# Kernel optimization log

Measured on AMD Instinct MI355X. Metric: run time of the kernel, lower is better.

The kernel has to match this reference:

```python
import jax, jax.numpy as jnp
import numpy as np

B, C, K, H, W = 32, 256, 64, 56, 56


def setup_inputs() -> dict:
    key = jax.random.key(0)
    k1, k2, k3, k4 = jax.random.split(key, 4)
    main_out = jax.random.normal(k1, (B, C, H, W), dtype=jnp.float32)
    dup_out = jax.random.normal(k2, (B, K, H, W), dtype=jnp.float32)
    # buffers: per-channel valid ranges with min <= max
    min_vals = -jnp.abs(jax.random.uniform(k3, (C,), dtype=jnp.float32))
    max_vals = jnp.abs(jax.random.uniform(k4, (C,), dtype=jnp.float32)) + 0.5
    vulnerable_idx = jnp.arange(K, dtype=jnp.int32)  # first K channels are duplicated
    return {
        "main_out": main_out,
        "dup_out": dup_out,
        "min_vals": min_vals,
        "max_vals": max_vals,
        "vulnerable_idx": vulnerable_idx,
    }


def reference(main_out, dup_out, min_vals, max_vals, vulnerable_idx):
    # nan->0 (inf handled like torch.nan_to_num defaults: clamped to finite max)
    main = jnp.nan_to_num(main_out, nan=0.0)
    dup = jnp.nan_to_num(dup_out, nan=0.0)

    lo = min_vals[None, :, None, None]   # [1,C,1,1]
    hi = max_vals[None, :, None, None]

    # non-vulnerable path: zero out-of-range values (applied to all channels,
    # then vulnerable channels are overwritten below)
    out = jnp.where((main >= lo) & (main <= hi), main, jnp.zeros((), main.dtype))

    # vulnerable channels: compare main vs duplicate
    m = main[:, vulnerable_idx]          # [B,K,H,W]
    d = dup                              # [B,K,H,W]
    lov = min_vals[vulnerable_idx][None, :, None, None]
    hiv = max_vals[vulnerable_idx][None, :, None, None]
    m_valid = (m >= lov) & (m <= hiv)
    d_valid = (d >= lov) & (d <= hiv)

    # both valid and differing -> min(m,d); only d valid -> d;
    # m valid (alone or both-equal) -> m; neither -> 0
    res = jnp.where(
        m_valid & d_valid & (m != d), jnp.minimum(m, d),
        jnp.where(d_valid & ~m_valid, d,
                  jnp.where(m_valid, m, jnp.zeros((), m.dtype))))

    return out.at[:, vulnerable_idx].set(res)
```

## Files before the change

kernel.cpp:

```cpp
#include <hip/hip_runtime.h>

constexpr int BB  = 32;
constexpr int CC  = 256;
constexpr int HWN = 56 * 56;
constexpr int HW4 = HWN / 4;

typedef float v4f __attribute__((ext_vector_type(4)));

__device__ __forceinline__ float edac_pair(float x, float y, float lo, float hi) {
    if (x != x) x = 0.0f;
    if (y != y) y = 0.0f;
    bool mv = (x >= lo) && (x <= hi);
    bool dv = (y >= lo) && (y <= hi);
    return (mv && dv && (x != y)) ? fminf(x, y)
         : ((dv && !mv) ? y
         : (mv ? x : 0.0f));
}

__device__ __forceinline__ float edac_single(float x, float lo, float hi) {
    if (x != x) x = 0.0f;
    bool mv = (x >= lo) && (x <= hi);
    return mv ? x : 0.0f;
}

__global__ __launch_bounds__(256) void edac_kernel(
    const float* __restrict__ mainp,
    const float* __restrict__ dupp,
    const float* __restrict__ lov,
    const float* __restrict__ hiv,
    const int*   __restrict__ vidx,
    float*       __restrict__ out,
    int K)
{
    const int bc = blockIdx.x;
    const int b  = bc >> 8;
    const int c  = bc & (CC - 1);
    const int t  = threadIdx.x;

    __shared__ int sk;
    if (t == 0) sk = -1;
    __syncthreads();
    if (t < K && vidx[t] == c) sk = t;
    __syncthreads();
    const int k = sk;

    const float lo = lov[c];
    const float hi = hiv[c];

    const v4f* mp = (const v4f*)(mainp + (size_t)bc * HWN);
    v4f*       op = (v4f*)(out   + (size_t)bc * HWN);

    const bool extra = (t < HW4 - 3 * 256);

    v4f m0 = mp[t];
    v4f m1 = mp[t + 256];
    v4f m2 = mp[t + 512];
    v4f m3 = extra ? mp[t + 768] : (v4f)(0.0f);

    if (k >= 0) {
        const v4f* dp = (const v4f*)(dupp + ((size_t)b * K + k) * HWN);
        v4f d0 = dp[t];
        v4f d1 = dp[t + 256];
        v4f d2 = dp[t + 512];
        v4f d3 = extra ? dp[t + 768] : (v4f)(0.0f);

        v4f r0, r1, r2, r3;
        #pragma unroll
        for (int e = 0; e < 4; ++e) {
            r0[e] = edac_pair(m0[e], d0[e], lo, hi);
            r1[e] = edac_pair(m1[e], d1[e], lo, hi);
            r2[e] = edac_pair(m2[e], d2[e], lo, hi);
            r3[e] = edac_pair(m3[e], d3[e], lo, hi);
        }
        __builtin_nontemporal_store(r0, &op[t]);
        __builtin_nontemporal_store(r1, &op[t + 256]);
        __builtin_nontemporal_store(r2, &op[t + 512]);
        if (extra) __builtin_nontemporal_store(r3, &op[t + 768]);
    } else {
        v4f r0, r1, r2, r3;
        #pragma unroll
        for (int e = 0; e < 4; ++e) {
            r0[e] = edac_single(m0[e], lo, hi);
            r1[e] = edac_single(m1[e], lo, hi);
            r2[e] = edac_single(m2[e], lo, hi);
            r3[e] = edac_single(m3[e], lo, hi);
        }
        __builtin_nontemporal_store(r0, &op[t]);
        __builtin_nontemporal_store(r1, &op[t + 256]);
        __builtin_nontemporal_store(r2, &op[t + 512]);
        if (extra) __builtin_nontemporal_store(r3, &op[t + 768]);
    }
}

extern "C" void kernel_launch(void* const* d_in, const int* in_sizes, int n_in,
                              void* d_out, int out_size, void* d_ws, size_t ws_size,
                              hipStream_t stream) {
    const float* mainp = (const float*)d_in[0];
    const float* dupp  = (const float*)d_in[1];
    const float* lov   = (const float*)d_in[2];
    const float* hiv   = (const float*)d_in[3];
    const int*   vidx  = (const int*)d_in[4];
    const int    K     = in_sizes[4];

    hipLaunchKernelGGL(edac_kernel, dim3(BB * CC), dim3(256), 0, stream,
                       mainp, dupp, lov, hiv, vidx, (float*)d_out, K);
}
```

Before: 206.3 us.

## Process four planes per block with software-prefetched nontemporal loads

```diff
diff --git a/kernel.cpp b/kernel.cpp
--- a/kernel.cpp
+++ b/kernel.cpp
@@ -4,6 +4,9 @@
 constexpr int CC  = 256;
 constexpr int HWN = 56 * 56;
 constexpr int HW4 = HWN / 4;
+
+constexpr int NPLANE = 4;
+constexpr int GRID   = BB * CC / NPLANE;
 
 typedef float v4f __attribute__((ext_vector_type(4)));
 
@@ -19,8 +22,25 @@
 
 __device__ __forceinline__ float edac_single(float x, float lo, float hi) {
     if (x != x) x = 0.0f;
-    bool mv = (x >= lo) && (x <= hi);
-    return mv ? x : 0.0f;
+    return ((x >= lo) && (x <= hi)) ? x : 0.0f;
+}
+
+__device__ __forceinline__ void load_plane(const float* p, int t, bool extra,
+                                           v4f& x0, v4f& x1, v4f& x2, v4f& x3) {
+    const v4f* vp = (const v4f*)p;
+    x0 = __builtin_nontemporal_load(&vp[t]);
+    x1 = __builtin_nontemporal_load(&vp[t + 256]);
+    x2 = __builtin_nontemporal_load(&vp[t + 512]);
+    x3 = extra ? __builtin_nontemporal_load(&vp[t + 768]) : (v4f)(0.0f);
+}
+
+__device__ __forceinline__ void store_plane(float* p, int t, bool extra,
+                                            v4f r0, v4f r1, v4f r2, v4f r3) {
+    v4f* vp = (v4f*)p;
+    __builtin_nontemporal_store(r0, &vp[t]);
+    __builtin_nontemporal_store(r1, &vp[t + 256]);
+    __builtin_nontemporal_store(r2, &vp[t + 512]);
+    if (extra) __builtin_nontemporal_store(r3, &vp[t + 768]);
 }
 
 __global__ __launch_bounds__(256) void edac_kernel(
@@ -32,10 +52,10 @@
     float*       __restrict__ out,
     int K)
 {
-    const int bc = blockIdx.x;
-    const int b  = bc >> 8;
-    const int c  = bc & (CC - 1);
-    const int t  = threadIdx.x;
+    const int bid = blockIdx.x;
+    const int c   = bid & (CC - 1);
+    const int b0  = bid >> 8;
+    const int t   = threadIdx.x;
 
     __shared__ int sk;
     if (t == 0) sk = -1;
@@ -46,49 +66,60 @@
 
     const float lo = lov[c];
     const float hi = hiv[c];
-
-    const v4f* mp = (const v4f*)(mainp + (size_t)bc * HWN);
-    v4f*       op = (v4f*)(out   + (size_t)bc * HWN);
-
     const bool extra = (t < HW4 - 3 * 256);
 
-    v4f m0 = mp[t];
-    v4f m1 = mp[t + 256];
-    v4f m2 = mp[t + 512];
-    v4f m3 = extra ? mp[t + 768] : (v4f)(0.0f);
+    const size_t step = (size_t)GRID * HWN;
+    const float* mb = mainp + (size_t)bid * HWN;
+    float*       ob = out   + (size_t)bid * HWN;
 
     if (k >= 0) {
-        const v4f* dp = (const v4f*)(dupp + ((size_t)b * K + k) * HWN);
-        v4f d0 = dp[t];
-        v4f d1 = dp[t + 256];
-        v4f d2 = dp[t + 512];
-        v4f d3 = extra ? dp[t + 768] : (v4f)(0.0f);
+        const size_t dstep = (size_t)(BB / NPLANE) * K * HWN;
+        const float* db = dupp + ((size_t)b0 * K + k) * HWN;
 
-        v4f r0, r1, r2, r3;
+        v4f a0, a1, a2, a3, da0, da1, da2, da3;
+        load_plane(mb, t, extra, a0, a1, a2, a3);
+        load_plane(db, t, extra, da0, da1, da2, da3);
+
         #pragma unroll
-        for (int e = 0; e < 4; ++e) {
-            r0[e] = edac_pair(m0[e], d0[e], lo, hi);
-            r1[e] = edac_pair(m1[e], d1[e], lo, hi);
-            r2[e] = edac_pair(m2[e], d2[e], lo, hi);
-            r3[e] = edac_pair(m3[e], d3[e], lo, hi);
+        for (int i = 0; i < NPLANE; ++i) {
+            v4f n0, n1, n2, n3, nd0, nd1, nd2, nd3;
+            if (i + 1 < NPLANE) {
+                load_plane(mb + (size_t)(i + 1) * step,  t, extra, n0, n1, n2, n3);
+                load_plane(db + (size_t)(i + 1) * dstep, t, extra, nd0, nd1, nd2, nd3);
+            }
+            v4f r0, r1, r2, r3;
+            #pragma unroll
+            for (int e = 0; e < 4; ++e) {
+                r0[e] = edac_pair(a0[e], da0[e], lo, hi);
+                r1[e] = edac_pair(a1[e], da1[e], lo, hi);
+                r2[e] = edac_pair(a2[e], da2[e], lo, hi);
+                r3[e] = edac_pair(a3[e], da3[e], lo, hi);
+            }
+            store_plane(ob + (size_t)i * step, t, extra, r0, r1, r2, r3);
+            a0 = n0; a1 = n1; a2 = n2; a3 = n3;
+            da0 = nd0; da1 = nd1; da2 = nd2; da3 = nd3;
         }
-        __builtin_nontemporal_store(r0, &op[t]);
-        __builtin_nontemporal_store(r1, &op[t + 256]);
-        __builtin_nontemporal_store(r2, &op[t + 512]);
-        if (extra) __builtin_nontemporal_store(r3, &op[t + 768]);
     } else {
-        v4f r0, r1, r2, r3;
+        v4f a0, a1, a2, a3;
+        load_plane(mb, t, extra, a0, a1, a2, a3);
+
         #pragma unroll
-        for (int e = 0; e < 4; ++e) {
-            r0[e] = edac_single(m0[e], lo, hi);
-            r1[e] = edac_single(m1[e], lo, hi);
-            r2[e] = edac_single(m2[e], lo, hi);
-            r3[e] = edac_single(m3[e], lo, hi);
+        for (int i = 0; i < NPLANE; ++i) {
+            v4f n0, n1, n2, n3;
+            if (i + 1 < NPLANE) {
+                load_plane(mb + (size_t)(i + 1) * step, t, extra, n0, n1, n2, n3);
+            }
+            v4f r0, r1, r2, r3;
+            #pragma unroll
+            for (int e = 0; e < 4; ++e) {
+                r0[e] = edac_single(a0[e], lo, hi);
+                r1[e] = edac_single(a1[e], lo, hi);
+                r2[e] = edac_single(a2[e], lo, hi);
+                r3[e] = edac_single(a3[e], lo, hi);
+            }
+            store_plane(ob + (size_t)i * step, t, extra, r0, r1, r2, r3);
+            a0 = n0; a1 = n1; a2 = n2; a3 = n3;
         }
-        __builtin_nontemporal_store(r0, &op[t]);
-        __builtin_nontemporal_store(r1, &op[t + 256]);
-        __builtin_nontemporal_store(r2, &op[t + 512]);
-        if (extra) __builtin_nontemporal_store(r3, &op[t + 768]);
     }
 }
 
@@ -102,6 +133,6 @@
     const int*   vidx  = (const int*)d_in[4];
     const int    K     = in_sizes[4];
 
-    hipLaunchKernelGGL(edac_kernel, dim3(BB * CC), dim3(256), 0, stream,
+    hipLaunchKernelGGL(edac_kernel, dim3(GRID), dim3(256), 0, stream,
                        mainp, dupp, lov, hiv, vidx, (float*)d_out, K);
 }
```

New measurement: 199.7 us. 1.03x faster.
